# Kernel optimization log

Hardware: AMD Instinct MI355X
Metric: run time of the kernel (lower is better)

The kernel has to match this reference:

```python
import jax, jax.numpy as jnp
import numpy as np

BATCH_SIZE = 2048   # init kwarg batch_size
MAX_ATOMS = 640     # static pad size; >= max atoms per molecule w.h.p. (mean 488, std ~22)
N_ATOMS = 1_000_000
D_FEAT = 64


def setup_inputs() -> dict:
    key = jax.random.key(0)
    k1, k2 = jax.random.split(key)
    atom_features = jax.random.normal(k1, (N_ATOMS, D_FEAT), dtype=jnp.float32)
    molecule_indicator = jnp.sort(
        jax.random.randint(k2, (N_ATOMS,), 0, BATCH_SIZE, dtype=jnp.int64)
    )
    return {"atom_features": atom_features, "molecule_indicator": molecule_indicator}


def reference(atom_features, molecule_indicator):
    # atom_features: [N, D] float; molecule_indicator: [N] int, sorted, values in [0, BATCH_SIZE)
    N, D = atom_features.shape
    # first atom index of each molecule (indicator is sorted)
    starts = jnp.searchsorted(molecule_indicator, jnp.arange(BATCH_SIZE))  # [B]
    # intra-molecule offset of each atom (replaces per-molecule boolean masking + pad)
    pos = jnp.arange(N) - starts[molecule_indicator]  # [N]
    # single fused scatter into the zero-padded dense batch (pad value = 0, as F.pad)
    stacked = jnp.zeros((BATCH_SIZE, MAX_ATOMS, D), dtype=atom_features.dtype)
    stacked = stacked.at[molecule_indicator, pos].set(atom_features)  # [B, MAX_ATOMS, D]
    # drop all-zero (empty) molecules; fixed-size nonzero keeps shapes static under jit.
    # With our inputs every molecule is non-empty, so this gather is the identity.
    nonempty = jnp.nonzero(stacked.sum(axis=(1, 2)) != 0, size=BATCH_SIZE, fill_value=0)[0]
    return stacked[nonempty]
```

## Files before the change

kernel.cpp:

```cpp
#include <hip/hip_runtime.h>


#define BATCH 2048
#define MAXA  640
#define DF    64

__global__ void pp_starts_kernel(const int* __restrict__ ind, int N,
                                 int* __restrict__ starts) {
    int m = blockIdx.x * blockDim.x + threadIdx.x;
    if (m > BATCH) return;
    if (m == BATCH) { starts[m] = N; return; }
    int lo = 0, hi = N;
    while (lo < hi) {
        int mid = (lo + hi) >> 1;
        if (ind[mid] < m) lo = mid + 1; else hi = mid;
    }
    starts[m] = lo;
}

__global__ void pp_gather_kernel(const float4* __restrict__ feat,
                                 const int* __restrict__ starts,
                                 float4* __restrict__ out) {
    const int m   = blockIdx.y;
    const int idx = blockIdx.x * blockDim.x + threadIdx.x;
    const int p   = idx >> 4;
    const int q   = idx & 15;
    const int s   = starts[m];
    const int e   = starts[m + 1];
    float4 v = make_float4(0.f, 0.f, 0.f, 0.f);
    const int src = s + p;
    if (src < e) v = feat[(long long)src * 16 + q];
    out[((long long)m * MAXA + p) * 16 + q] = v;
}

extern "C" void kernel_launch(void* const* d_in, const int* in_sizes, int n_in,
                              void* d_out, int out_size, void* d_ws, size_t ws_size,
                              hipStream_t stream) {
    const float* feat = (const float*)d_in[0];
    const int*   ind  = (const int*)d_in[1];
    float*       out  = (float*)d_out;
    int*         starts = (int*)d_ws;

    const int N = in_sizes[0] / DF;

    {
        dim3 grid((BATCH + 1 + 255) / 256);
        pp_starts_kernel<<<grid, 256, 0, stream>>>(ind, N, starts);
    }

    {
        dim3 grid(MAXA * (DF / 4) / 256, BATCH);
        pp_gather_kernel<<<grid, 256, 0, stream>>>(
            (const float4*)feat, starts, (float4*)out);
    }
}
```

Measured before the change: 112.9 us.

## Compute molecule starts by boundary scan and gather two rows per thread

Replaces the per-molecule binary search with a grid-stride scan over the sorted indicator that writes each start where the molecule id changes. The gather kernel now handles two atom rows per thread (offset 320) with 32-bit index math, halving the grid. The goal is to cut serialized dependent loads in the starts kernel and reduce per-thread overhead in the memory-bound gather, at the cost of reading the whole indicator array once.

```diff
diff --git a/kernel.cpp b/kernel.cpp
--- a/kernel.cpp
+++ b/kernel.cpp
@@ -7,30 +7,41 @@
 
 __global__ void pp_starts_kernel(const int* __restrict__ ind, int N,
                                  int* __restrict__ starts) {
-    int m = blockIdx.x * blockDim.x + threadIdx.x;
-    if (m > BATCH) return;
-    if (m == BATCH) { starts[m] = N; return; }
-    int lo = 0, hi = N;
-    while (lo < hi) {
-        int mid = (lo + hi) >> 1;
-        if (ind[mid] < m) lo = mid + 1; else hi = mid;
+    int stride = gridDim.x * blockDim.x;
+    for (int i = blockIdx.x * blockDim.x + threadIdx.x; i < N; i += stride) {
+        int cur  = ind[i];
+        int prev = (i == 0) ? -1 : ind[i - 1];
+        if (cur != prev) {
+            for (int m = prev + 1; m <= cur; ++m) starts[m] = i;
+        }
+        if (i == N - 1) {
+            for (int m = cur + 1; m <= BATCH; ++m) starts[m] = N;
+        }
     }
-    starts[m] = lo;
 }
 
-__global__ void pp_gather_kernel(const float4* __restrict__ feat,
-                                 const int* __restrict__ starts,
-                                 float4* __restrict__ out) {
-    const int m   = blockIdx.y;
-    const int idx = blockIdx.x * blockDim.x + threadIdx.x;
-    const int p   = idx >> 4;
-    const int q   = idx & 15;
-    const int s   = starts[m];
-    const int e   = starts[m + 1];
-    float4 v = make_float4(0.f, 0.f, 0.f, 0.f);
-    const int src = s + p;
-    if (src < e) v = feat[(long long)src * 16 + q];
-    out[((long long)m * MAXA + p) * 16 + q] = v;
+__global__ __launch_bounds__(256) void pp_gather_kernel(
+        const float4* __restrict__ feat,
+        const int* __restrict__ starts,
+        float4* __restrict__ out) {
+    const unsigned m   = blockIdx.y;
+    const unsigned idx = blockIdx.x * 256u + threadIdx.x;
+    const unsigned p0  = idx >> 4;
+    const unsigned q   = idx & 15u;
+    const int s = starts[m];
+    const int e = starts[m + 1];
+
+    const unsigned src0 = (unsigned)s + p0;
+    const unsigned src1 = src0 + 320u;
+
+    float4 v0 = make_float4(0.f, 0.f, 0.f, 0.f);
+    float4 v1 = make_float4(0.f, 0.f, 0.f, 0.f);
+    if ((int)src0 < e) v0 = feat[src0 * 16u + q];
+    if ((int)src1 < e) v1 = feat[src1 * 16u + q];
+
+    const unsigned obase = m * (MAXA * 16u) + p0 * 16u + q;
+    out[obase]            = v0;
+    out[obase + 320u*16u] = v1;
 }
 
 extern "C" void kernel_launch(void* const* d_in, const int* in_sizes, int n_in,
@@ -44,12 +55,12 @@
     const int N = in_sizes[0] / DF;
 
     {
-        dim3 grid((BATCH + 1 + 255) / 256);
-        pp_starts_kernel<<<grid, 256, 0, stream>>>(ind, N, starts);
+        int blocks = min((N + 255) / 256, 4096);
+        pp_starts_kernel<<<blocks, 256, 0, stream>>>(ind, N, starts);
     }
 
     {
-        dim3 grid(MAXA * (DF / 4) / 256, BATCH);
+        dim3 grid(MAXA * (DF / 4) / (2 * 256), BATCH);
         pp_gather_kernel<<<grid, 256, 0, stream>>>(
             (const float4*)feat, starts, (float4*)out);
     }
```

New measurement: 114.5 us. Within noise of the previous version (+1.4%).

## Fuse start search into gather kernel with four float4s per thread

Applied to the files above, without the earlier changes.

Drops the separate starts kernel and its workspace round-trip. Each gather block now runs two binary searches over the sorted indicator to find its molecule's start and end. Each thread copies four float4 rows-chunks instead of one, giving 10 blocks per molecule instead of 40, and indexing uses 32-bit unsigned math. The cost is redundant binary searches per block (about 20 dependent loads each, mostly cache hits), and the 32-bit indices could overflow on larger inputs.

```diff
diff --git a/kernel.cpp b/kernel.cpp
--- a/kernel.cpp
+++ b/kernel.cpp
@@ -4,33 +4,47 @@
 #define BATCH 2048
 #define MAXA  640
 #define DF    64
+#define ROWF4 16
 
-__global__ void pp_starts_kernel(const int* __restrict__ ind, int N,
-                                 int* __restrict__ starts) {
-    int m = blockIdx.x * blockDim.x + threadIdx.x;
-    if (m > BATCH) return;
-    if (m == BATCH) { starts[m] = N; return; }
+typedef float f4 __attribute__((ext_vector_type(4)));
+
+__global__ __launch_bounds__(256) void pp_fused_kernel(
+        const f4* __restrict__ feat,
+        const int* __restrict__ ind,
+        f4* __restrict__ out,
+        int N) {
+    const int m = blockIdx.y;
+
     int lo = 0, hi = N;
     while (lo < hi) {
         int mid = (lo + hi) >> 1;
         if (ind[mid] < m) lo = mid + 1; else hi = mid;
     }
-    starts[m] = lo;
-}
+    const int s = lo;
+    hi = N;
+    while (lo < hi) {
+        int mid = (lo + hi) >> 1;
+        if (ind[mid] < m + 1) lo = mid + 1; else hi = mid;
+    }
+    const int e = lo;
 
-__global__ void pp_gather_kernel(const float4* __restrict__ feat,
-                                 const int* __restrict__ starts,
-                                 float4* __restrict__ out) {
-    const int m   = blockIdx.y;
-    const int idx = blockIdx.x * blockDim.x + threadIdx.x;
-    const int p   = idx >> 4;
-    const int q   = idx & 15;
-    const int s   = starts[m];
-    const int e   = starts[m + 1];
-    float4 v = make_float4(0.f, 0.f, 0.f, 0.f);
-    const int src = s + p;
-    if (src < e) v = feat[(long long)src * 16 + q];
-    out[((long long)m * MAXA + p) * 16 + q] = v;
+    const unsigned base = blockIdx.x * 1024u + threadIdx.x;
+
+    f4 v0 = (f4){0.f,0.f,0.f,0.f}, v1 = v0, v2 = v0, v3 = v0;
+    {
+        const unsigned r0 = base, r1 = base + 256u, r2 = base + 512u, r3 = base + 768u;
+        const unsigned fb = (unsigned)s * ROWF4;
+        if (s + (int)(r0 >> 4) < e) v0 = feat[fb + r0];
+        if (s + (int)(r1 >> 4) < e) v1 = feat[fb + r1];
+        if (s + (int)(r2 >> 4) < e) v2 = feat[fb + r2];
+        if (s + (int)(r3 >> 4) < e) v3 = feat[fb + r3];
+    }
+
+    f4* o = out + (unsigned)m * (MAXA * ROWF4);
+    o[base]        = v0;
+    o[base + 256u] = v1;
+    o[base + 512u] = v2;
+    o[base + 768u] = v3;
 }
 
 extern "C" void kernel_launch(void* const* d_in, const int* in_sizes, int n_in,
@@ -39,18 +53,10 @@
     const float* feat = (const float*)d_in[0];
     const int*   ind  = (const int*)d_in[1];
     float*       out  = (float*)d_out;
-    int*         starts = (int*)d_ws;
 
     const int N = in_sizes[0] / DF;
 
-    {
-        dim3 grid((BATCH + 1 + 255) / 256);
-        pp_starts_kernel<<<grid, 256, 0, stream>>>(ind, N, starts);
-    }
-
-    {
-        dim3 grid(MAXA * (DF / 4) / 256, BATCH);
-        pp_gather_kernel<<<grid, 256, 0, stream>>>(
-            (const float4*)feat, starts, (float4*)out);
-    }
+    dim3 grid(MAXA * ROWF4 / 1024, BATCH);
+    pp_fused_kernel<<<grid, 256, 0, stream>>>(
+        (const f4*)feat, ind, (f4*)out, N);
 }
```

Result: slower. 149.9 us (+32.8%).
